# Optimization experiments

Hardware: AMD Instinct MI355X
Metric: run time of the kernel (lower is better)

Reference implementation:

```python
import jax, jax.numpy as jnp
import numpy as np

B, L, D = 2, 2048, 2048
H, KVH, HD, FD = 8, 1, 256, 64   # heads, kv heads, head_dim, feature_dim
CHUNK = 64


def setup_inputs() -> dict:
    key = jax.random.key(0)
    ks = jax.random.split(key, 8)
    hidden_states = jax.random.normal(ks[0], (B, L, D), dtype=jnp.float32)
    # Gemma-style RoPE tables over half the head dim
    half = HD // 2
    inv_freq = 1.0 / (10000.0 ** (jnp.arange(half, dtype=jnp.float32) / half))
    ang = jnp.arange(L, dtype=jnp.float32)[:, None] * inv_freq[None, :]  # [L, half]
    freqs_cos, freqs_sin = jnp.cos(ang), jnp.sin(ang)
    mask = jnp.ones((1, 1, L, L), dtype=bool)  # unused in linear path
    s = 0.02
    Wq = jax.random.normal(ks[1], (D, H * HD), dtype=jnp.float32) * s
    Wk = jax.random.normal(ks[2], (D, KVH * HD), dtype=jnp.float32) * s
    Wv = jax.random.normal(ks[3], (D, KVH * HD), dtype=jnp.float32) * s
    Wo = jax.random.normal(ks[4], (H * HD, D), dtype=jnp.float32) * s
    fmq = jax.random.normal(ks[5], (H, HD, FD), dtype=jnp.float32) * s
    fmk = jax.random.normal(ks[6], (H, HD, FD), dtype=jnp.float32) * s
    return dict(hidden_states=hidden_states, freqs_cos=freqs_cos, freqs_sin=freqs_sin,
                mask=mask, Wq=Wq, Wk=Wk, Wv=Wv, Wo=Wo, fmq=fmq, fmk=fmk)


def _rope(x, cos, sin):
    # x: [B, L, h, HD]; Gemma complex RoPE: first half = real, second half = imag
    half = x.shape[-1] // 2
    x1, x2 = x[..., :half], x[..., half:]
    c = cos[None, :, None, :]
    s = sin[None, :, None, :]
    return jnp.concatenate([x1 * c - x2 * s, x1 * s + x2 * c], axis=-1)


def _hedgehog(x, W):
    # x: [B, H, L, HD], W: [H, HD, FD] -> softmax over cat([xW, -xW]) -> [B,H,L,2*FD]
    p = jnp.einsum('bhld,hdf->bhlf', x, W)
    return jax.nn.softmax(jnp.concatenate([p, -p], axis=-1), axis=-1)


def _chunk_linear_attn(q, k, v, chunk=CHUNK):
    # q,k: [B,H,L,F]; v: [B,H,L,HD]; chunked causal linear attention
    b, h, l, f = q.shape
    dv = v.shape[-1]
    n = l // chunk
    q = q.reshape(b, h, n, chunk, f) * (f ** -0.5)
    k = k.reshape(b, h, n, chunk, f)
    v = v.reshape(b, h, n, chunk, dv)
    kv = jnp.einsum('bhncf,bhncd->bhnfd', k, v)            # per-chunk KV
    kv = jnp.cumsum(kv, axis=2)
    kv = jnp.concatenate([jnp.zeros_like(kv[:, :, :1]), kv[:, :, :-1]], axis=2)  # exclusive prefix
    inter = jnp.einsum('bhncf,bhnfd->bhncd', q, kv)        # cross-chunk term
    s = jnp.einsum('bhnif,bhnjf->bhnij', q, k)             # intra-chunk scores
    tri = jnp.tril(jnp.ones((chunk, chunk), dtype=bool))
    s = jnp.where(tri, s, 0.0)
    intra = jnp.einsum('bhnij,bhnjd->bhnid', s, v)
    return (inter + intra).reshape(b, h, l, dv)


def reference(hidden_states, freqs_cos, freqs_sin, mask, Wq, Wk, Wv, Wo, fmq, fmk):
    b, l, _ = hidden_states.shape
    q = (hidden_states @ Wq).reshape(b, l, H, HD)
    k = (hidden_states @ Wk).reshape(b, l, KVH, HD)
    v = (hidden_states @ Wv).reshape(b, l, KVH, HD)
    q = _rope(q, freqs_cos, freqs_sin)
    k = _rope(k, freqs_cos, freqs_sin)
    # repeat_interleave kv heads to num_heads (MQA expansion)
    rep = H // KVH
    k = jnp.repeat(k, rep, axis=2)
    v = jnp.repeat(v, rep, axis=2)
    q = jnp.transpose(q, (0, 2, 1, 3))  # [B,H,L,HD]
    k = jnp.transpose(k, (0, 2, 1, 3))
    v = jnp.transpose(v, (0, 2, 1, 3))
    q = _hedgehog(q, fmq)
    k = _hedgehog(k, fmk)
    o = _chunk_linear_attn(q, k, v)                         # [B,H,L,HD]
    o = jnp.transpose(o, (0, 2, 1, 3)).reshape(b, l, H * HD)
    return o @ Wo
```

## Files before the change

### kernel.cpp

```cpp
#include <hip/hip_runtime.h>

#define B_ 2
#define L_ 2048
#define D_ 2048
#define H_ 8
#define HD_ 256
#define FD_ 64
#define F_ 128
#define NC_ 32
#define M_ (B_*L_)
#define SCALE_Q 0.08838834764831845f

typedef unsigned short u16;
typedef __attribute__((ext_vector_type(8))) short bf16x8;
typedef __attribute__((ext_vector_type(8))) unsigned short u16x8;
typedef __attribute__((ext_vector_type(16))) float f32x16;

#define FMA4(a_, s_, v_) { (a_).x += (s_)*(v_).x; (a_).y += (s_)*(v_).y; \
                           (a_).z += (s_)*(v_).z; (a_).w += (s_)*(v_).w; }


__device__ __forceinline__ u16 bf16_rne(float x) {
  unsigned u = __float_as_uint(x);
  return (u16)((u + 0x7fffu + ((u >> 16) & 1u)) >> 16);
}
__device__ __forceinline__ void bf16_split(float x, u16& h, u16& l) {
  unsigned u = __float_as_uint(x);
  unsigned hb = (u + 0x7fffu + ((u >> 16) & 1u)) >> 16;
  h = (u16)hb;
  float hf = __uint_as_float(hb << 16);
  l = bf16_rne(x - hf);
}

__device__ __forceinline__ void gl_lds16(const u16* g, u16* l) {
  __builtin_amdgcn_global_load_lds(
      (const __attribute__((address_space(1))) unsigned int*)g,
      (__attribute__((address_space(3))) unsigned int*)l, 16, 0, 0);
}

__global__ __launch_bounds__(256)
void split_tiled(const float* __restrict__ x, u16* __restrict__ th,
                 u16* __restrict__ tl) {
  int gid = blockIdx.x * 256 + threadIdx.x;
  int r = gid >> 8, u = gid & 255;
  const float* src = x + (size_t)r * 2048 + u * 8;
  float4 v0 = *(const float4*)src, v1 = *(const float4*)(src + 4);
  float vals[8] = {v0.x, v0.y, v0.z, v0.w, v1.x, v1.y, v1.z, v1.w};
  u16x8 hv, lv;
  #pragma unroll
  for (int j = 0; j < 8; ++j) { u16 hh, ll; bf16_split(vals[j], hh, ll); hv[j] = hh; lv[j] = ll; }
  size_t off = ((size_t)(r >> 6) * 64 + (u >> 2)) * 2048
             + (size_t)((u >> 1) & 1) * 1024 + (size_t)((r >> 5) & 1) * 512
             + (size_t)(u & 1) * 256 + (size_t)(r & 31) * 8;
  *(u16x8*)(th + off) = hv;
  *(u16x8*)(tl + off) = lv;
}

__device__ __forceinline__ void wtrans_body(const float* __restrict__ W, int Nsrc,
                                            int n0, u16* __restrict__ dst,
                                            int P, int kt) {
  int t = threadIdx.x;
  int nn = t & 127, kh = t >> 7;
  const float* src = W + (size_t)(kt * 32 + kh * 16) * Nsrc + n0 + nn;
  u16x8 u0, u1;
  #pragma unroll
  for (int kk = 0; kk < 8; ++kk) u0[kk] = bf16_rne(src[(size_t)kk * Nsrc]);
  #pragma unroll
  for (int kk = 0; kk < 8; ++kk) u1[kk] = bf16_rne(src[(size_t)(kk + 8) * Nsrc]);
  size_t base = ((size_t)P * 64 + kt) * 4096 + (size_t)((nn >> 6) & 1) * 2048
              + (size_t)kh * 1024 + (size_t)((nn >> 5) & 1) * 512
              + (size_t)(nn & 31) * 8;
  *(u16x8*)(dst + base) = u0;
  *(u16x8*)(dst + base + 256) = u1;
}

__global__ __launch_bounds__(256)
void wtrans_qkv(const float* __restrict__ Wq, const float* __restrict__ Wk,
                const float* __restrict__ Wv, u16* __restrict__ WTh) {
  int P = blockIdx.x, kt = blockIdx.y;
  const float* W; int Nsrc, n0;
  if (P < 16)      { W = Wq; Nsrc = 2048; n0 = P * 128; }
  else if (P < 18) { W = Wk; Nsrc = 256;  n0 = (P - 16) * 128; }
  else             { W = Wv; Nsrc = 256;  n0 = (P - 18) * 128; }
  wtrans_body(W, Nsrc, n0, WTh, P, kt);
}

__global__ __launch_bounds__(256)
void wtrans_wo(const float* __restrict__ Wo, u16* __restrict__ WoTh) {
  wtrans_body(Wo, 2048, blockIdx.x * 128, WoTh, blockIdx.x, blockIdx.y);
}

__device__ __forceinline__ void mfma_body(
    const u16* __restrict__ AtH, const u16* __restrict__ AtL,
    const u16* __restrict__ Bt, float* __restrict__ C, int cstride,
    int bm, int bn) {
  __shared__ __align__(16) u16 AsH[2048];
  __shared__ __align__(16) u16 AsL[2048];
  __shared__ __align__(16) u16 Bs[4096];
  const int t = threadIdx.x, lane = t & 63, wv = t >> 6;
  const u16* aSrc = (wv ? AtL : AtH) + (size_t)bm * 131072 + lane * 8;
  const u16* bSrc = Bt + (size_t)bn * 262144 + wv * 2048 + lane * 8;
  u16* aDst = wv ? AsL : AsH;
  u16* bDst = Bs + wv * 2048;

  f32x16 acc[2][2];
  #pragma unroll
  for (int a = 0; a < 2; ++a)
    #pragma unroll
    for (int b2 = 0; b2 < 2; ++b2)
      #pragma unroll
      for (int r = 0; r < 16; ++r) acc[a][b2][r] = 0.f;

  for (int kt = 0; kt < 64; ++kt) {
    const u16* ak = aSrc + (size_t)kt * 2048;
    const u16* bk = bSrc + (size_t)kt * 4096;
    __syncthreads();
    #pragma unroll
    for (int c = 0; c < 4; ++c) {
      gl_lds16(ak + c * 512, aDst + c * 512);
      gl_lds16(bk + c * 512, bDst + c * 512);
    }
    __syncthreads();

    #pragma unroll
    for (int ks = 0; ks < 2; ++ks) {
      const u16* ph = AsH + ks * 1024 + lane * 8;
      const u16* pl = AsL + ks * 1024 + lane * 8;
      const u16* pb = Bs + wv * 2048 + ks * 1024 + lane * 8;
      bf16x8 a0 = *(const bf16x8*)ph;
      bf16x8 a1 = *(const bf16x8*)(ph + 512);
      bf16x8 b0 = *(const bf16x8*)pb;
      bf16x8 b1 = *(const bf16x8*)(pb + 512);
      acc[0][0] = __builtin_amdgcn_mfma_f32_32x32x16_bf16(a0, b0, acc[0][0], 0, 0, 0);
      acc[0][1] = __builtin_amdgcn_mfma_f32_32x32x16_bf16(a0, b1, acc[0][1], 0, 0, 0);
      acc[1][0] = __builtin_amdgcn_mfma_f32_32x32x16_bf16(a1, b0, acc[1][0], 0, 0, 0);
      acc[1][1] = __builtin_amdgcn_mfma_f32_32x32x16_bf16(a1, b1, acc[1][1], 0, 0, 0);
      bf16x8 l0 = *(const bf16x8*)pl;
      bf16x8 l1 = *(const bf16x8*)(pl + 512);
      acc[0][0] = __builtin_amdgcn_mfma_f32_32x32x16_bf16(l0, b0, acc[0][0], 0, 0, 0);
      acc[0][1] = __builtin_amdgcn_mfma_f32_32x32x16_bf16(l0, b1, acc[0][1], 0, 0, 0);
      acc[1][0] = __builtin_amdgcn_mfma_f32_32x32x16_bf16(l1, b0, acc[1][0], 0, 0, 0);
      acc[1][1] = __builtin_amdgcn_mfma_f32_32x32x16_bf16(l1, b1, acc[1][1], 0, 0, 0);
    }
  }

  const int fr = lane & 31, g = lane >> 5;
  float* Cp = C + (size_t)(bm * 64) * cstride + wv * 64;
  #pragma unroll
  for (int mt = 0; mt < 2; ++mt)
    #pragma unroll
    for (int nt = 0; nt < 2; ++nt) {
      #pragma unroll
      for (int r = 0; r < 16; ++r) {
        int row = mt * 32 + (r & 3) + 8 * (r >> 2) + 4 * g;
        Cp[(size_t)row * cstride + nt * 32 + fr] = acc[mt][nt][r];
      }
    }
}

__global__ __launch_bounds__(128, 4)
void mfma_qkv(const u16* __restrict__ hsHt, const u16* __restrict__ hsLt,
              const u16* __restrict__ WTh,
              float* __restrict__ q, float* __restrict__ k, float* __restrict__ v) {
  int bn = blockIdx.x, bm = blockIdx.y;
  float* Cb; int cs, co;
  if (bn < 16)      { Cb = q; cs = 2048; co = bn * 128; }
  else if (bn < 18) { Cb = k; cs = 256;  co = (bn - 16) * 128; }
  else              { Cb = v; cs = 256;  co = (bn - 18) * 128; }
  mfma_body(hsHt, hsLt, WTh, Cb + co, cs, bm, bn);
}

__global__ __launch_bounds__(128, 4)
void mfma_wo(const u16* __restrict__ oHt, const u16* __restrict__ oLt,
             const u16* __restrict__ WoTh, float* __restrict__ out) {
  mfma_body(oHt, oLt, WoTh, out + blockIdx.x * 128, 2048, blockIdx.y, blockIdx.x);
}

__device__ __forceinline__ float wave_max64(float v) {
  #pragma unroll
  for (int off = 32; off > 0; off >>= 1) v = fmaxf(v, __shfl_xor(v, off, 64));
  return v;
}
__device__ __forceinline__ float wave_sum64(float v) {
  #pragma unroll
  for (int off = 32; off > 0; off >>= 1) v += __shfl_xor(v, off, 64);
  return v;
}

__global__ __launch_bounds__(256)
void hedgehog_kernel(const float* __restrict__ x, const float* __restrict__ fm,
                     const float* __restrict__ cosb, const float* __restrict__ sinb,
                     float* __restrict__ out, int nh_in) {
  __shared__ __align__(16) float rows[4][4][256];
  int wave = threadIdx.x >> 6, lane = threadIdx.x & 63;
  int g = blockIdx.x * 4 + wave;
  int l4 = g & (L_/4 - 1);
  int bh = g / (L_/4);
  int h = bh & 7, b = bh >> 3;
  int l0 = l4 * 4;
  size_t rstride = (nh_in == 1) ? (size_t)HD_ : (size_t)H_ * HD_;
  const float* xrow = (nh_in == 1)
      ? x + (size_t)(b * L_ + l0) * HD_
      : x + ((size_t)(b * L_ + l0) * H_ + h) * HD_;
  int dd = (lane & 31) * 4;
  #pragma unroll
  for (int r = 0; r < 4; ++r) {
    float4 v = *(const float4*)(xrow + r * rstride + lane * 4);
    float4 u;
    u.x = __shfl_xor(v.x, 32, 64); u.y = __shfl_xor(v.y, 32, 64);
    u.z = __shfl_xor(v.z, 32, 64); u.w = __shfl_xor(v.w, 32, 64);
    int l = l0 + r;
    float4 c = *(const float4*)(cosb + (size_t)l * 128 + dd);
    float4 s = *(const float4*)(sinb + (size_t)l * 128 + dd);
    float4 ro;
    if (lane < 32) {
      ro.x = v.x * c.x - u.x * s.x; ro.y = v.y * c.y - u.y * s.y;
      ro.z = v.z * c.z - u.z * s.z; ro.w = v.w * c.w - u.w * s.w;
    } else {
      ro.x = u.x * s.x + v.x * c.x; ro.y = u.y * s.y + v.y * c.y;
      ro.z = u.z * s.z + v.z * c.z; ro.w = u.w * s.w + v.w * c.w;
    }
    *(float4*)&rows[wave][r][lane * 4] = ro;
  }
  __syncthreads();

  const float* fmh = fm + (size_t)h * HD_ * FD_;
  float p0 = 0.f, p1 = 0.f, p2 = 0.f, p3 = 0.f;
  for (int d2 = 0; d2 < HD_; d2 += 4) {
    float w0 = fmh[(d2 + 0) * FD_ + lane];
    float w1 = fmh[(d2 + 1) * FD_ + lane];
    float w2 = fmh[(d2 + 2) * FD_ + lane];
    float w3 = fmh[(d2 + 3) * FD_ + lane];
    float4 r0 = *(const float4*)&rows[wave][0][d2];
    float4 r1 = *(const float4*)&rows[wave][1][d2];
    float4 r2 = *(const float4*)&rows[wave][2][d2];
    float4 r3 = *(const float4*)&rows[wave][3][d2];
    p0 += r0.x * w0 + r0.y * w1 + r0.z * w2 + r0.w * w3;
    p1 += r1.x * w0 + r1.y * w1 + r1.z * w2 + r1.w * w3;
    p2 += r2.x * w0 + r2.y * w1 + r2.z * w2 + r2.w * w3;
    p3 += r3.x * w0 + r3.y * w1 + r3.z * w2 + r3.w * w3;
  }
  float p[4] = {p0, p1, p2, p3};
  #pragma unroll
  for (int r = 0; r < 4; ++r) {
    float m = wave_max64(fabsf(p[r]));
    float e1 = __expf(p[r] - m);
    float e2 = __expf(-p[r] - m);
    float z = wave_sum64(e1 + e2);
    float inv = 1.0f / z;
    size_t base = ((size_t)bh * L_ + l0 + r) * F_;
    out[base + lane]      = e1 * inv;
    out[base + 64 + lane] = e2 * inv;
  }
}

__global__ __launch_bounds__(256)
void chunk_kv_kernel(const float* __restrict__ kf, const float* __restrict__ v,
                     float* __restrict__ kvc) {
  __shared__ __align__(16) float kfs[64][128];
  int n = blockIdx.x & (NC_ - 1), bh = blockIdx.x >> 5;
  int b = bh >> 3;
  const float* kfp = kf + ((size_t)bh * L_ + (size_t)n * 64) * F_;
  int t = threadIdx.x;
  #pragma unroll
  for (int it = 0; it < 8; ++it) {
    int flat = t * 4 + it * 1024;
    *(float4*)&kfs[flat >> 7][flat & 127] = *(const float4*)(kfp + flat);
  }
  __syncthreads();
  int dg = t & 63;
  int fg = t >> 6;
  const float* vp = v + (size_t)(b * L_ + n * 64) * HD_ + dg * 4;
  float* outp = kvc + (size_t)blockIdx.x * (F_ * HD_) + dg * 4;
  #pragma unroll
  for (int pass = 0; pass < 4; ++pass) {
    int f0 = fg * 8 + pass * 32;
    float4 acc[8];
    #pragma unroll
    for (int i = 0; i < 8; ++i) acc[i] = make_float4(0.f, 0.f, 0.f, 0.f);
    for (int j = 0; j < 64; ++j) {
      float4 vv = *(const float4*)(vp + (size_t)j * HD_);
      float4 ka = *(const float4*)&kfs[j][f0];
      float4 kb = *(const float4*)&kfs[j][f0 + 4];
      FMA4(acc[0], ka.x, vv); FMA4(acc[1], ka.y, vv);
      FMA4(acc[2], ka.z, vv); FMA4(acc[3], ka.w, vv);
      FMA4(acc[4], kb.x, vv); FMA4(acc[5], kb.y, vv);
      FMA4(acc[6], kb.z, vv); FMA4(acc[7], kb.w, vv);
    }
    #pragma unroll
    for (int ff = 0; ff < 8; ++ff)
      *(float4*)(outp + (size_t)(f0 + ff) * HD_) = acc[ff];
  }
}

__global__ __launch_bounds__(256)
void chunk_scan_kernel(float* __restrict__ kvc) {
  size_t c = (size_t)blockIdx.x * 256 + threadIdx.x;
  size_t bh = c >> 15;
  size_t fd = c & 32767;
  float* p = kvc + bh * ((size_t)NC_ * F_ * HD_) + fd;
  float run = 0.f;
  #pragma unroll
  for (int n = 0; n < NC_; ++n) {
    float val = p[(size_t)n * (F_ * HD_)];
    p[(size_t)n * (F_ * HD_)] = run;
    run += val;
  }
}

__global__ __launch_bounds__(512)
void chunk_attn_kernel(const float* __restrict__ qf, const float* __restrict__ kf,
                       const float* __restrict__ v, const float* __restrict__ kvc,
                       u16* __restrict__ oHt, u16* __restrict__ oLt) {
  __shared__ __align__(16) float qsT[128][68];
  __shared__ __align__(16) float ksT[128][68];
  __shared__ __align__(16) float ssT[64][68];
  int n = blockIdx.x & (NC_ - 1), bh = blockIdx.x >> 5;
  int h = bh & 7, b = bh >> 3;
  int t = threadIdx.x;
  const float* qp = qf + ((size_t)bh * L_ + (size_t)n * 64) * F_;
  const float* kp = kf + ((size_t)bh * L_ + (size_t)n * 64) * F_;
  #pragma unroll
  for (int it = 0; it < 4; ++it) {
    int flat = t * 4 + it * 2048;
    int j = flat >> 7, f = flat & 127;
    float4 qv = *(const float4*)(qp + flat);
    qsT[f + 0][j] = qv.x * SCALE_Q; qsT[f + 1][j] = qv.y * SCALE_Q;
    qsT[f + 2][j] = qv.z * SCALE_Q; qsT[f + 3][j] = qv.w * SCALE_Q;
    float4 kv_ = *(const float4*)(kp + flat);
    ksT[f + 0][j] = kv_.x; ksT[f + 1][j] = kv_.y;
    ksT[f + 2][j] = kv_.z; ksT[f + 3][j] = kv_.w;
  }
  __syncthreads();

  if (t < 256) {
    int j4 = (t & 15) * 4, i4 = (t >> 4) * 4;
    float4 accs[4];
    #pragma unroll
    for (int i = 0; i < 4; ++i) accs[i] = make_float4(0.f, 0.f, 0.f, 0.f);
    for (int f = 0; f < F_; ++f) {
      float4 a4 = *(const float4*)&qsT[f][i4];
      float4 b4 = *(const float4*)&ksT[f][j4];
      FMA4(accs[0], a4.x, b4); FMA4(accs[1], a4.y, b4);
      FMA4(accs[2], a4.z, b4); FMA4(accs[3], a4.w, b4);
    }
    #pragma unroll
    for (int ii = 0; ii < 4; ++ii) {
      float sv[4] = {accs[ii].x, accs[ii].y, accs[ii].z, accs[ii].w};
      #pragma unroll
      for (int jj = 0; jj < 4; ++jj) {
        int i = i4 + ii, j = j4 + jj;
        ssT[j][i] = (j <= i) ? sv[jj] : 0.f;
      }
    }
  }
  __syncthreads();

  int dgrp = t & 31, rs = t >> 5;
  int d0 = dgrp * 8;
  const float* kvp = kvc + (size_t)blockIdx.x * (F_ * HD_) + d0;
  const float* vp = v + (size_t)(b * L_ + n * 64) * HD_ + d0;
  float4 acc[4][2];
  #pragma unroll
  for (int i = 0; i < 4; ++i) {
    acc[i][0] = make_float4(0.f, 0.f, 0.f, 0.f);
    acc[i][1] = make_float4(0.f, 0.f, 0.f, 0.f);
  }
  for (int f = 0; f < F_; ++f) {
    float4 kv0 = *(const float4*)(kvp + (size_t)f * HD_);
    float4 kv1 = *(const float4*)(kvp + (size_t)f * HD_ + 4);
    float4 a4 = *(const float4*)&qsT[f][rs * 4];
    FMA4(acc[0][0], a4.x, kv0); FMA4(acc[0][1], a4.x, kv1);
    FMA4(acc[1][0], a4.y, kv0); FMA4(acc[1][1], a4.y, kv1);
    FMA4(acc[2][0], a4.z, kv0); FMA4(acc[2][1], a4.z, kv1);
    FMA4(acc[3][0], a4.w, kv0); FMA4(acc[3][1], a4.w, kv1);
  }
  for (int j = 0; j < 64; ++j) {
    float4 v0 = *(const float4*)(vp + (size_t)j * HD_);
    float4 v1 = *(const float4*)(vp + (size_t)j * HD_ + 4);
    float4 s4 = *(const float4*)&ssT[j][rs * 4];
    FMA4(acc[0][0], s4.x, v0); FMA4(acc[0][1], s4.x, v1);
    FMA4(acc[1][0], s4.y, v0); FMA4(acc[1][1], s4.y, v1);
    FMA4(acc[2][0], s4.z, v0); FMA4(acc[2][1], s4.z, v1);
    FMA4(acc[3][0], s4.w, v0); FMA4(acc[3][1], s4.w, v1);
  }
  int p = (b * L_ + n * 64) >> 6;
  size_t obase = ((size_t)p * 64 + h * 8 + (dgrp >> 2)) * 2048
               + (size_t)((dgrp >> 1) & 1) * 1024 + (size_t)(dgrp & 1) * 256;
  #pragma unroll
  for (int ii = 0; ii < 4; ++ii) {
    int i = rs * 4 + ii;
    size_t off = obase + (size_t)((i >> 5) & 1) * 512 + (size_t)(i & 31) * 8;
    float vals[8] = {acc[ii][0].x, acc[ii][0].y, acc[ii][0].z, acc[ii][0].w,
                     acc[ii][1].x, acc[ii][1].y, acc[ii][1].z, acc[ii][1].w};
    u16x8 hv, lv;
    #pragma unroll
    for (int jj = 0; jj < 8; ++jj) { u16 hh, ll; bf16_split(vals[jj], hh, ll); hv[jj] = hh; lv[jj] = ll; }
    *(u16x8*)(oHt + off) = hv;
    *(u16x8*)(oLt + off) = lv;
  }
}

extern "C" void kernel_launch(void* const* d_in, const int* in_sizes, int n_in,
                              void* d_out, int out_size, void* d_ws, size_t ws_size,
                              hipStream_t stream) {
  const float* hs   = (const float*)d_in[0];
  const float* fcos = (const float*)d_in[1];
  const float* fsin = (const float*)d_in[2];
  const float* Wq  = (const float*)d_in[4];
  const float* Wk  = (const float*)d_in[5];
  const float* Wv  = (const float*)d_in[6];
  const float* Wo  = (const float*)d_in[7];
  const float* fmq = (const float*)d_in[8];
  const float* fmk = (const float*)d_in[9];
  float* out = (float*)d_out;

  float* ws = (float*)d_ws;
  float* q  = ws;
  float* k  = q  + (size_t)M_ * 2048;
  float* v  = k  + (size_t)M_ * 256;
  float* qf = v  + (size_t)M_ * 256;
  float* kf = qf + (size_t)B_ * H_ * L_ * F_;
  float* kv = kf + (size_t)B_ * H_ * L_ * F_;

  u16* hsHt = (u16*)kv;
  u16* hsLt = hsHt + (size_t)M_ * 2048;
  u16* WTh  = hsLt + (size_t)M_ * 2048;
  u16* WoTh = (u16*)kv;
  u16* oHt  = (u16*)q;
  u16* oLt  = oHt + (size_t)M_ * 2048;

  wtrans_qkv<<<dim3(20, 64), 256, 0, stream>>>(Wq, Wk, Wv, WTh);
  split_tiled<<<(M_ * 2048 / 8) / 256, 256, 0, stream>>>(hs, hsHt, hsLt);
  mfma_qkv<<<dim3(20, 64), 128, 0, stream>>>(hsHt, hsLt, WTh, q, k, v);
  hedgehog_kernel<<<(B_ * H_ * L_) / 16, 256, 0, stream>>>(q, fmq, fcos, fsin, qf, H_);
  hedgehog_kernel<<<(B_ * H_ * L_) / 16, 256, 0, stream>>>(k, fmk, fcos, fsin, kf, 1);
  chunk_kv_kernel<<<B_ * H_ * NC_, 256, 0, stream>>>(kf, v, kv);
  chunk_scan_kernel<<<(B_ * H_ * F_ * HD_) / 256, 256, 0, stream>>>(kv);
  chunk_attn_kernel<<<B_ * H_ * NC_, 512, 0, stream>>>(qf, kf, v, kv, oHt, oLt);
  wtrans_wo<<<dim3(16, 64), 256, 0, stream>>>(Wo, WoTh);
  mfma_wo<<<dim3(16, 64), 128, 0, stream>>>(oHt, oLt, WoTh, out);
}
```

Before: 538.7 us.

## Merge prep and hedgehog launches, deepen GEMM K-step, remap attention output threads

The hidden-state split and the QKV weight transpose now run as one launch, and the q and k hedgehog passes are merged into a single launch, removing two kernel launches. The bf16 GEMM body stages two K-tiles per barrier pair, doubling LDS use and halving the number of sync iterations. The chunk attention epilogue remaps threads so each handles two rows and 16 contiguous columns, changing the global read and store pattern. Larger LDS use per block may lower occupancy in the GEMMs.

```diff
diff --git a/kernel.cpp b/kernel.cpp
--- a/kernel.cpp
+++ b/kernel.cpp
@@ -38,24 +38,6 @@
       (__attribute__((address_space(3))) unsigned int*)l, 16, 0, 0);
 }
 
-__global__ __launch_bounds__(256)
-void split_tiled(const float* __restrict__ x, u16* __restrict__ th,
-                 u16* __restrict__ tl) {
-  int gid = blockIdx.x * 256 + threadIdx.x;
-  int r = gid >> 8, u = gid & 255;
-  const float* src = x + (size_t)r * 2048 + u * 8;
-  float4 v0 = *(const float4*)src, v1 = *(const float4*)(src + 4);
-  float vals[8] = {v0.x, v0.y, v0.z, v0.w, v1.x, v1.y, v1.z, v1.w};
-  u16x8 hv, lv;
-  #pragma unroll
-  for (int j = 0; j < 8; ++j) { u16 hh, ll; bf16_split(vals[j], hh, ll); hv[j] = hh; lv[j] = ll; }
-  size_t off = ((size_t)(r >> 6) * 64 + (u >> 2)) * 2048
-             + (size_t)((u >> 1) & 1) * 1024 + (size_t)((r >> 5) & 1) * 512
-             + (size_t)(u & 1) * 256 + (size_t)(r & 31) * 8;
-  *(u16x8*)(th + off) = hv;
-  *(u16x8*)(tl + off) = lv;
-}
-
 __device__ __forceinline__ void wtrans_body(const float* __restrict__ W, int Nsrc,
                                             int n0, u16* __restrict__ dst,
                                             int P, int kt) {
@@ -75,14 +57,35 @@
 }
 
 __global__ __launch_bounds__(256)
-void wtrans_qkv(const float* __restrict__ Wq, const float* __restrict__ Wk,
-                const float* __restrict__ Wv, u16* __restrict__ WTh) {
-  int P = blockIdx.x, kt = blockIdx.y;
-  const float* W; int Nsrc, n0;
-  if (P < 16)      { W = Wq; Nsrc = 2048; n0 = P * 128; }
-  else if (P < 18) { W = Wk; Nsrc = 256;  n0 = (P - 16) * 128; }
-  else             { W = Wv; Nsrc = 256;  n0 = (P - 18) * 128; }
-  wtrans_body(W, Nsrc, n0, WTh, P, kt);
+void prep_kernel(const float* __restrict__ hs,
+                 const float* __restrict__ Wq, const float* __restrict__ Wk,
+                 const float* __restrict__ Wv,
+                 u16* __restrict__ hsHt, u16* __restrict__ hsLt,
+                 u16* __restrict__ WTh) {
+  int bid = blockIdx.x;
+  if (bid < 4096) {
+    int gid = bid * 256 + threadIdx.x;
+    int r = gid >> 8, u = gid & 255;
+    const float* src = hs + (size_t)r * 2048 + u * 8;
+    float4 v0 = *(const float4*)src, v1 = *(const float4*)(src + 4);
+    float vals[8] = {v0.x, v0.y, v0.z, v0.w, v1.x, v1.y, v1.z, v1.w};
+    u16x8 hv, lv;
+    #pragma unroll
+    for (int j = 0; j < 8; ++j) { u16 hh, ll; bf16_split(vals[j], hh, ll); hv[j] = hh; lv[j] = ll; }
+    size_t off = ((size_t)(r >> 6) * 64 + (u >> 2)) * 2048
+               + (size_t)((u >> 1) & 1) * 1024 + (size_t)((r >> 5) & 1) * 512
+               + (size_t)(u & 1) * 256 + (size_t)(r & 31) * 8;
+    *(u16x8*)(hsHt + off) = hv;
+    *(u16x8*)(hsLt + off) = lv;
+  } else {
+    int idx = bid - 4096;
+    int P = idx >> 6, kt = idx & 63;
+    const float* W; int Nsrc, n0;
+    if (P < 16)      { W = Wq; Nsrc = 2048; n0 = P * 128; }
+    else if (P < 18) { W = Wk; Nsrc = 256;  n0 = (P - 16) * 128; }
+    else             { W = Wv; Nsrc = 256;  n0 = (P - 18) * 128; }
+    wtrans_body(W, Nsrc, n0, WTh, P, kt);
+  }
 }
 
 __global__ __launch_bounds__(256)
@@ -94,9 +97,9 @@
     const u16* __restrict__ AtH, const u16* __restrict__ AtL,
     const u16* __restrict__ Bt, float* __restrict__ C, int cstride,
     int bm, int bn) {
-  __shared__ __align__(16) u16 AsH[2048];
-  __shared__ __align__(16) u16 AsL[2048];
-  __shared__ __align__(16) u16 Bs[4096];
+  __shared__ __align__(16) u16 AsH[4096];
+  __shared__ __align__(16) u16 AsL[4096];
+  __shared__ __align__(16) u16 Bs[8192];
   const int t = threadIdx.x, lane = t & 63, wv = t >> 6;
   const u16* aSrc = (wv ? AtL : AtH) + (size_t)bm * 131072 + lane * 8;
   const u16* bSrc = Bt + (size_t)bn * 262144 + wv * 2048 + lane * 8;
@@ -111,22 +114,25 @@
       #pragma unroll
       for (int r = 0; r < 16; ++r) acc[a][b2][r] = 0.f;
 
-  for (int kt = 0; kt < 64; ++kt) {
-    const u16* ak = aSrc + (size_t)kt * 2048;
-    const u16* bk = bSrc + (size_t)kt * 4096;
+  for (int it = 0; it < 32; ++it) {
+    const u16* ak = aSrc + (size_t)it * 4096;
+    const u16* bk = bSrc + (size_t)it * 8192;
     __syncthreads();
     #pragma unroll
+    for (int c = 0; c < 8; ++c)
+      gl_lds16(ak + c * 512, aDst + c * 512);
+    #pragma unroll
     for (int c = 0; c < 4; ++c) {
-      gl_lds16(ak + c * 512, aDst + c * 512);
       gl_lds16(bk + c * 512, bDst + c * 512);
+      gl_lds16(bk + 4096 + c * 512, bDst + 4096 + c * 512);
     }
     __syncthreads();
 
     #pragma unroll
-    for (int ks = 0; ks < 2; ++ks) {
-      const u16* ph = AsH + ks * 1024 + lane * 8;
-      const u16* pl = AsL + ks * 1024 + lane * 8;
-      const u16* pb = Bs + wv * 2048 + ks * 1024 + lane * 8;
+    for (int ks = 0; ks < 4; ++ks) {
+      const u16* ph = AsH + (ks >> 1) * 2048 + (ks & 1) * 1024 + lane * 8;
+      const u16* pl = AsL + (ks >> 1) * 2048 + (ks & 1) * 1024 + lane * 8;
+      const u16* pb = Bs + (ks >> 1) * 4096 + wv * 2048 + (ks & 1) * 1024 + lane * 8;
       bf16x8 a0 = *(const bf16x8*)ph;
       bf16x8 a1 = *(const bf16x8*)(ph + 512);
       bf16x8 b0 = *(const bf16x8*)pb;
@@ -188,12 +194,17 @@
 }
 
 __global__ __launch_bounds__(256)
-void hedgehog_kernel(const float* __restrict__ x, const float* __restrict__ fm,
+void hedgehog_kernel(const float* __restrict__ q, const float* __restrict__ kx,
+                     const float* __restrict__ fmq, const float* __restrict__ fmk,
                      const float* __restrict__ cosb, const float* __restrict__ sinb,
-                     float* __restrict__ out, int nh_in) {
+                     float* __restrict__ qf, float* __restrict__ kf) {
   __shared__ __align__(16) float rows[4][4][256];
+  int bid = blockIdx.x;
+  const float* x; const float* fm; float* out; int nh_in, gb;
+  if (bid < 2048) { x = q;  fm = fmq; out = qf; nh_in = 8; gb = bid * 4; }
+  else            { x = kx; fm = fmk; out = kf; nh_in = 1; gb = (bid - 2048) * 4; }
   int wave = threadIdx.x >> 6, lane = threadIdx.x & 63;
-  int g = blockIdx.x * 4 + wave;
+  int g = gb + wave;
   int l4 = g & (L_/4 - 1);
   int bh = g / (L_/4);
   int h = bh & 7, b = bh >> 3;
@@ -356,48 +367,52 @@
   }
   __syncthreads();
 
-  int dgrp = t & 31, rs = t >> 5;
-  int d0 = dgrp * 8;
+  int il = t & 31, dg = t >> 5;
+  int d0 = dg * 16;
   const float* kvp = kvc + (size_t)blockIdx.x * (F_ * HD_) + d0;
   const float* vp = v + (size_t)(b * L_ + n * 64) * HD_ + d0;
-  float4 acc[4][2];
-  #pragma unroll
-  for (int i = 0; i < 4; ++i) {
-    acc[i][0] = make_float4(0.f, 0.f, 0.f, 0.f);
-    acc[i][1] = make_float4(0.f, 0.f, 0.f, 0.f);
-  }
+  float4 acc[2][4];
+  #pragma unroll
+  for (int rh = 0; rh < 2; ++rh)
+    #pragma unroll
+    for (int c = 0; c < 4; ++c) acc[rh][c] = make_float4(0.f, 0.f, 0.f, 0.f);
+
   for (int f = 0; f < F_; ++f) {
-    float4 kv0 = *(const float4*)(kvp + (size_t)f * HD_);
-    float4 kv1 = *(const float4*)(kvp + (size_t)f * HD_ + 4);
-    float4 a4 = *(const float4*)&qsT[f][rs * 4];
-    FMA4(acc[0][0], a4.x, kv0); FMA4(acc[0][1], a4.x, kv1);
-    FMA4(acc[1][0], a4.y, kv0); FMA4(acc[1][1], a4.y, kv1);
-    FMA4(acc[2][0], a4.z, kv0); FMA4(acc[2][1], a4.z, kv1);
-    FMA4(acc[3][0], a4.w, kv0); FMA4(acc[3][1], a4.w, kv1);
+    float qa = qsT[f][il], qb = qsT[f][il + 32];
+    const float* kr = kvp + (size_t)f * HD_;
+    float4 k0 = *(const float4*)kr, k1 = *(const float4*)(kr + 4);
+    float4 k2 = *(const float4*)(kr + 8), k3 = *(const float4*)(kr + 12);
+    FMA4(acc[0][0], qa, k0); FMA4(acc[0][1], qa, k1);
+    FMA4(acc[0][2], qa, k2); FMA4(acc[0][3], qa, k3);
+    FMA4(acc[1][0], qb, k0); FMA4(acc[1][1], qb, k1);
+    FMA4(acc[1][2], qb, k2); FMA4(acc[1][3], qb, k3);
   }
   for (int j = 0; j < 64; ++j) {
-    float4 v0 = *(const float4*)(vp + (size_t)j * HD_);
-    float4 v1 = *(const float4*)(vp + (size_t)j * HD_ + 4);
-    float4 s4 = *(const float4*)&ssT[j][rs * 4];
-    FMA4(acc[0][0], s4.x, v0); FMA4(acc[0][1], s4.x, v1);
-    FMA4(acc[1][0], s4.y, v0); FMA4(acc[1][1], s4.y, v1);
-    FMA4(acc[2][0], s4.z, v0); FMA4(acc[2][1], s4.z, v1);
-    FMA4(acc[3][0], s4.w, v0); FMA4(acc[3][1], s4.w, v1);
+    float sa = ssT[j][il], sb = ssT[j][il + 32];
+    const float* vr = vp + (size_t)j * HD_;
+    float4 v0 = *(const float4*)vr, v1 = *(const float4*)(vr + 4);
+    float4 v2 = *(const float4*)(vr + 8), v3 = *(const float4*)(vr + 12);
+    FMA4(acc[0][0], sa, v0); FMA4(acc[0][1], sa, v1);
+    FMA4(acc[0][2], sa, v2); FMA4(acc[0][3], sa, v3);
+    FMA4(acc[1][0], sb, v0); FMA4(acc[1][1], sb, v1);
+    FMA4(acc[1][2], sb, v2); FMA4(acc[1][3], sb, v3);
   }
   int p = (b * L_ + n * 64) >> 6;
-  size_t obase = ((size_t)p * 64 + h * 8 + (dgrp >> 2)) * 2048
-               + (size_t)((dgrp >> 1) & 1) * 1024 + (size_t)(dgrp & 1) * 256;
-  #pragma unroll
-  for (int ii = 0; ii < 4; ++ii) {
-    int i = rs * 4 + ii;
-    size_t off = obase + (size_t)((i >> 5) & 1) * 512 + (size_t)(i & 31) * 8;
-    float vals[8] = {acc[ii][0].x, acc[ii][0].y, acc[ii][0].z, acc[ii][0].w,
-                     acc[ii][1].x, acc[ii][1].y, acc[ii][1].z, acc[ii][1].w};
-    u16x8 hv, lv;
-    #pragma unroll
-    for (int jj = 0; jj < 8; ++jj) { u16 hh, ll; bf16_split(vals[jj], hh, ll); hv[jj] = hh; lv[jj] = ll; }
-    *(u16x8*)(oHt + off) = hv;
-    *(u16x8*)(oLt + off) = lv;
+  size_t base0 = ((size_t)p * 64 + h * 8 + (dg >> 1)) * 2048
+               + (size_t)(dg & 1) * 1024;
+  #pragma unroll
+  for (int rh = 0; rh < 2; ++rh) {
+    #pragma unroll
+    for (int uu = 0; uu < 2; ++uu) {
+      float4 lo = acc[rh][uu * 2], hi = acc[rh][uu * 2 + 1];
+      float vals[8] = {lo.x, lo.y, lo.z, lo.w, hi.x, hi.y, hi.z, hi.w};
+      u16x8 hv, lv;
+      #pragma unroll
+      for (int jj = 0; jj < 8; ++jj) { u16 hh, ll; bf16_split(vals[jj], hh, ll); hv[jj] = hh; lv[jj] = ll; }
+      size_t off = base0 + (size_t)rh * 512 + (size_t)uu * 256 + (size_t)il * 8;
+      *(u16x8*)(oHt + off) = hv;
+      *(u16x8*)(oLt + off) = lv;
+    }
   }
 }
 
@@ -430,11 +445,9 @@
   u16* oHt  = (u16*)q;
   u16* oLt  = oHt + (size_t)M_ * 2048;
 
-  wtrans_qkv<<<dim3(20, 64), 256, 0, stream>>>(Wq, Wk, Wv, WTh);
-  split_tiled<<<(M_ * 2048 / 8) / 256, 256, 0, stream>>>(hs, hsHt, hsLt);
+  prep_kernel<<<4096 + 1280, 256, 0, stream>>>(hs, Wq, Wk, Wv, hsHt, hsLt, WTh);
   mfma_qkv<<<dim3(20, 64), 128, 0, stream>>>(hsHt, hsLt, WTh, q, k, v);
-  hedgehog_kernel<<<(B_ * H_ * L_) / 16, 256, 0, stream>>>(q, fmq, fcos, fsin, qf, H_);
-  hedgehog_kernel<<<(B_ * H_ * L_) / 16, 256, 0, stream>>>(k, fmk, fcos, fsin, kf, 1);
+  hedgehog_kernel<<<2048 + 2048, 256, 0, stream>>>(q, k, fmq, fmk, fcos, fsin, qf, kf);
   chunk_kv_kernel<<<B_ * H_ * NC_, 256, 0, stream>>>(kf, v, kv);
   chunk_scan_kernel<<<(B_ * H_ * F_ * HD_) / 256, 256, 0, stream>>>(kv);
   chunk_attn_kernel<<<B_ * H_ * NC_, 512, 0, stream>>>(qf, kf, v, kv, oHt, oLt);
```

Result: slower. 580.6 us (+7.8%).
